# Kernel tuning notes

Measured on AMD Instinct MI355X. Metric: run time of the kernel, lower is better.

The kernel has to match this reference:

```python
import jax, jax.numpy as jnp
import numpy as np

B, S, D, H, FF = 1, 4096, 512, 8, 2048
DK = D // H
EPS = 1e-6


def layer_norm(x, alpha, beta):
    # Original LayerNorm: scalar alpha/beta, torch.std (ddof=1), eps added to std.
    mean = jnp.mean(x, axis=-1, keepdims=True)
    var = jnp.var(x, axis=-1, keepdims=True) * (D / (D - 1))  # Bessel-corrected, like torch.std
    std = jnp.sqrt(var)
    return alpha * (x - mean) / (std + EPS) + beta


def setup_inputs() -> dict:
    key = jax.random.key(0)
    ks = jax.random.split(key, 12)
    sd = 1.0 / np.sqrt(D)
    sf = 1.0 / np.sqrt(FF)
    inp = {
        "x": jax.random.normal(ks[0], (B, S, D), jnp.float32),
        "mask": jnp.ones((1, 1, 1, S), jnp.int32),
        "wq": jax.random.uniform(ks[1], (D, D), jnp.float32, -sd, sd),
        "bq": jnp.zeros((D,), jnp.float32),
        "wk": jax.random.uniform(ks[2], (D, D), jnp.float32, -sd, sd),
        "bk": jnp.zeros((D,), jnp.float32),
        "wv": jax.random.uniform(ks[3], (D, D), jnp.float32, -sd, sd),
        "bv": jnp.zeros((D,), jnp.float32),
        "wo": jax.random.uniform(ks[4], (D, D), jnp.float32, -sd, sd),
        "bo": jnp.zeros((D,), jnp.float32),
        "w1": jax.random.uniform(ks[5], (D, FF), jnp.float32, -sd, sd),
        "b1": jnp.zeros((FF,), jnp.float32),
        "w2": jax.random.uniform(ks[6], (FF, D), jnp.float32, -sf, sf),
        "b2": jnp.zeros((D,), jnp.float32),
        "ln1_a": jnp.ones((1,), jnp.float32),
        "ln1_b": jnp.zeros((1,), jnp.float32),
        "ln2_a": jnp.ones((1,), jnp.float32),
        "ln2_b": jnp.zeros((1,), jnp.float32),
    }
    return inp


def reference(x, mask, wq, bq, wk, bk, wv, bv, wo, bo, w1, b1, w2, b2,
              ln1_a, ln1_b, ln2_a, ln2_b):
    # --- pre-LN self-attention sublayer with residual ---
    h = layer_norm(x, ln1_a, ln1_b)
    q = (h @ wq + bq).reshape(B, S, H, DK).transpose(0, 2, 1, 3)  # [B,H,S,dk]
    k = (h @ wk + bk).reshape(B, S, H, DK).transpose(0, 2, 1, 3)
    v = (h @ wv + bv).reshape(B, S, H, DK).transpose(0, 2, 1, 3)
    scores = jnp.einsum('bhqd,bhkd->bhqk', q, k) / np.sqrt(DK)     # [B,H,S,S]
    scores = jnp.where(mask == 0, jnp.float32(-1e9), scores)
    probs = jax.nn.softmax(scores, axis=-1)
    attn = jnp.einsum('bhqk,bhkd->bhqd', probs, v)                 # [B,H,S,dk]
    attn = attn.transpose(0, 2, 1, 3).reshape(B, S, D)
    x = x + (attn @ wo + bo)
    # --- pre-LN feed-forward sublayer with residual ---
    h2 = layer_norm(x, ln2_a, ln2_b)
    ff = jax.nn.relu(h2 @ w1 + b1) @ w2 + b2
    return x + ff
```

## Files before the change

### kernel.cpp

```cpp
#include <hip/hip_runtime.h>
#include <hip/hip_bf16.h>

#define S_LEN 4096
#define D_DIM 512
#define H_NUM 8
#define DK_DIM 64
#define FF_DIM 2048
#define QLD 1536

typedef __attribute__((ext_vector_type(8))) short short8;
typedef __attribute__((ext_vector_type(4))) float f32x4;
typedef __attribute__((ext_vector_type(4))) ushort us4;

#if __has_builtin(__builtin_amdgcn_exp2f)
#define EXP2F __builtin_amdgcn_exp2f
#else
#define EXP2F exp2f
#endif

__device__ __forceinline__ ushort f2bf(float f) {
    union { float f; uint u; } v; v.f = f;
    uint r = v.u + 0x7FFF + ((v.u >> 16) & 1);
    return (ushort)(r >> 16);
}

__device__ __forceinline__ void gload_lds16(const void* g, void* l) {
    __builtin_amdgcn_global_load_lds(
        (const __attribute__((address_space(1))) void*)g,
        (__attribute__((address_space(3))) void*)l,
        16, 0, 0);
}

#define MFMA16(a, b, c) __builtin_amdgcn_mfma_f32_16x16x32_bf16(a, b, c, 0, 0, 0)

__global__ __launch_bounds__(256) void prep_all(
    const float* __restrict__ wq, const float* __restrict__ wk,
    const float* __restrict__ wv, const float* __restrict__ wo,
    const float* __restrict__ w1, const float* __restrict__ w2,
    const float* __restrict__ bq, const float* __restrict__ bk,
    const float* __restrict__ bv, const int* __restrict__ mask,
    ushort* __restrict__ wqkvt, ushort* __restrict__ wot,
    ushort* __restrict__ w1t, ushort* __restrict__ w2t,
    float* __restrict__ bqkv, float* __restrict__ mbias)
{
    __shared__ float t[32][33];
    const int bid = blockIdx.x, tid = threadIdx.x;
    if (bid < 3072) {
        const float* src; ushort* dst; int K, N, tx, ty;
        if (bid < 1024) {
            int wsel = bid >> 8, id = bid & 255;
            src = wsel == 0 ? wq : wsel == 1 ? wk : wsel == 2 ? wv : wo;
            dst = wsel == 0 ? wqkvt : wsel == 1 ? wqkvt + 512 * 512
                : wsel == 2 ? wqkvt + 1024 * 512 : wot;
            K = 512; N = 512; tx = id & 15; ty = id >> 4;
        } else if (bid < 2048) {
            int id = bid - 1024; src = w1; dst = w1t;
            K = 512; N = 2048; tx = id & 63; ty = id >> 6;
        } else {
            int id = bid - 2048; src = w2; dst = w2t;
            K = 2048; N = 512; tx = id & 15; ty = id >> 4;
        }
        int gn = tx * 32, gk = ty * 32;
        int lx = tid & 31, ly = tid >> 5;
#pragma unroll
        for (int i = 0; i < 32; i += 8)
            t[ly + i][lx] = src[(size_t)(gk + ly + i) * N + gn + lx];
        __syncthreads();
#pragma unroll
        for (int i = 0; i < 32; i += 8)
            dst[(size_t)(gn + ly + i) * K + gk + lx] = f2bf(t[lx][ly + i]);
    } else {
        int i = (bid - 3072) * 256 + tid;
        if (i < 512)       bqkv[i] = bq[i];
        else if (i < 1024) bqkv[i] = bk[i - 512];
        else if (i < 1536) bqkv[i] = bv[i - 1024];
        mbias[i] = mask[i] ? 0.0f : -1e9f;
    }
}

__global__ __launch_bounds__(256) void ln1_kernel(
    const float* __restrict__ x,
    const float* __restrict__ aP, const float* __restrict__ bP,
    ushort* __restrict__ out)
{
    const int row = blockIdx.x;
    const int d = threadIdx.x * 2;
    float2 v = *(const float2*)(x + (size_t)row * D_DIM + d);
    float sum = v.x + v.y;
    float sq  = v.x * v.x + v.y * v.y;
#pragma unroll
    for (int off = 1; off < 64; off <<= 1) {
        sum += __shfl_xor(sum, off);
        sq  += __shfl_xor(sq, off);
    }
    __shared__ float ssum[4], ssq[4];
    int wid = threadIdx.x >> 6;
    if ((threadIdx.x & 63) == 0) { ssum[wid] = sum; ssq[wid] = sq; }
    __syncthreads();
    sum = ssum[0] + ssum[1] + ssum[2] + ssum[3];
    sq  = ssq[0] + ssq[1] + ssq[2] + ssq[3];
    float mean = sum * (1.0f / D_DIM);
    float var  = (sq - (float)D_DIM * mean * mean) * (1.0f / (D_DIM - 1));
    var = fmaxf(var, 0.0f);
    float scale = aP[0] / (sqrtf(var) + 1e-6f);
    float beta  = bP[0];
    ushort2 o;
    o.x = f2bf((v.x - mean) * scale + beta);
    o.y = f2bf((v.y - mean) * scale + beta);
    *(ushort2*)(out + (size_t)row * D_DIM + d) = o;
}

__global__ __launch_bounds__(256) void ln2_fused(
    const float* __restrict__ x, const float* __restrict__ bo,
    const float* __restrict__ p0, const float* __restrict__ p1,
    const float* __restrict__ aP, const float* __restrict__ bP,
    float* __restrict__ x2, ushort* __restrict__ h2)
{
    const int row = blockIdx.x;
    const int d = threadIdx.x * 2;
    const size_t idx = (size_t)row * D_DIM + d;
    float2 xv = *(const float2*)(x + idx);
    float2 a0 = *(const float2*)(p0 + idx);
    float2 a1 = *(const float2*)(p1 + idx);
    float2 bb = *(const float2*)(bo + d);
    float2 v;
    v.x = xv.x + a0.x + a1.x + bb.x;
    v.y = xv.y + a0.y + a1.y + bb.y;
    *(float2*)(x2 + idx) = v;
    float sum = v.x + v.y;
    float sq  = v.x * v.x + v.y * v.y;
#pragma unroll
    for (int off = 1; off < 64; off <<= 1) {
        sum += __shfl_xor(sum, off);
        sq  += __shfl_xor(sq, off);
    }
    __shared__ float ssum[4], ssq[4];
    int wid = threadIdx.x >> 6;
    if ((threadIdx.x & 63) == 0) { ssum[wid] = sum; ssq[wid] = sq; }
    __syncthreads();
    sum = ssum[0] + ssum[1] + ssum[2] + ssum[3];
    sq  = ssq[0] + ssq[1] + ssq[2] + ssq[3];
    float mean = sum * (1.0f / D_DIM);
    float var  = (sq - (float)D_DIM * mean * mean) * (1.0f / (D_DIM - 1));
    var = fmaxf(var, 0.0f);
    float scale = aP[0] / (sqrtf(var) + 1e-6f);
    float beta  = bP[0];
    ushort2 o;
    o.x = f2bf((v.x - mean) * scale + beta);
    o.y = f2bf((v.y - mean) * scale + beta);
    *(ushort2*)(h2 + idx) = o;
}

__global__ __launch_bounds__(256) void gemm_mfma(
    const ushort* __restrict__ A, const ushort* __restrict__ Bt,
    const float* __restrict__ bias,
    float* __restrict__ outF, ushort* __restrict__ outB,
    ushort* __restrict__ outVT,
    int M, int N, int K, int relu, int ksl)
{
    __shared__ ushort As[2][2][128][32];
    __shared__ ushort Bs[2][2][64][32];
    const int tid = threadIdx.x;
    const int w = tid >> 6, lane = tid & 63;
    const int l15 = lane & 15, quad = lane >> 4;
    const int sw = (l15 >> 1) & 3;
    const int swc = ((lane & 3) ^ ((lane >> 3) & 3)) * 16;
    const int m0 = blockIdx.y * 128, n0 = blockIdx.x * 64;
    const int kz = blockIdx.z;
    const int kbeg = kz * ksl;

    f32x4 acc[2][4] = {};

    const char* gA  = (const char*)(A  + (size_t)(m0 + 32 * w + (lane >> 2)) * K + kbeg) + swc;
    const char* gA2 = gA + (size_t)16 * K * 2;
    const char* gB  = (const char*)(Bt + (size_t)(n0 + 16 * w + (lane >> 2)) * K + kbeg) + swc;

    auto stage = [&](int b) {
        gload_lds16(gA,       &As[b][0][32 * w][0]);
        gload_lds16(gA + 64,  &As[b][1][32 * w][0]);
        gload_lds16(gA2,      &As[b][0][32 * w + 16][0]);
        gload_lds16(gA2 + 64, &As[b][1][32 * w + 16][0]);
        gload_lds16(gB,       &Bs[b][0][16 * w][0]);
        gload_lds16(gB + 64,  &Bs[b][1][16 * w][0]);
        gA += 128; gA2 += 128; gB += 128;
    };

    stage(0);
    const int nit = ksl >> 6;
    for (int t = 0; t < nit; ++t) {
        __syncthreads();
        if (t + 1 < nit) stage((t + 1) & 1);
        const int b = t & 1;
#pragma unroll
        for (int ks = 0; ks < 2; ++ks) {
            short8 a0 = *(const short8*)&As[b][ks][32 * w + l15][(quad ^ sw) * 8];
            short8 a1 = *(const short8*)&As[b][ks][32 * w + 16 + l15][(quad ^ sw) * 8];
            short8 b0 = *(const short8*)&Bs[b][ks][0 * 16 + l15][(quad ^ sw) * 8];
            short8 b1 = *(const short8*)&Bs[b][ks][1 * 16 + l15][(quad ^ sw) * 8];
            short8 b2 = *(const short8*)&Bs[b][ks][2 * 16 + l15][(quad ^ sw) * 8];
            short8 b3 = *(const short8*)&Bs[b][ks][3 * 16 + l15][(quad ^ sw) * 8];
            acc[0][0] = MFMA16(a0, b0, acc[0][0]);
            acc[0][1] = MFMA16(a0, b1, acc[0][1]);
            acc[0][2] = MFMA16(a0, b2, acc[0][2]);
            acc[0][3] = MFMA16(a0, b3, acc[0][3]);
            acc[1][0] = MFMA16(a1, b0, acc[1][0]);
            acc[1][1] = MFMA16(a1, b1, acc[1][1]);
            acc[1][2] = MFMA16(a1, b2, acc[1][2]);
            acc[1][3] = MFMA16(a1, b3, acc[1][3]);
        }
    }

    if (ksl < K) {
        float* of = outF + (size_t)kz * M * N;
#pragma unroll
        for (int mt = 0; mt < 2; ++mt)
#pragma unroll
            for (int nt = 0; nt < 4; ++nt)
#pragma unroll
                for (int r = 0; r < 4; ++r) {
                    int mm = m0 + 32 * w + mt * 16 + quad * 4 + r;
                    int nn = n0 + nt * 16 + l15;
                    of[(size_t)mm * N + nn] = acc[mt][nt][r];
                }
        return;
    }

    if (outVT && n0 >= 1024) {
#pragma unroll
        for (int mt = 0; mt < 2; ++mt)
#pragma unroll
            for (int nt = 0; nt < 4; ++nt) {
                int nn = n0 + nt * 16 + l15;
                int mmb = m0 + 32 * w + mt * 16 + quad * 4;
                us4 pk;
#pragma unroll
                for (int r = 0; r < 4; ++r)
                    pk[r] = (short)f2bf(acc[mt][nt][r] + bias[nn]);
                *(us4*)(outVT + (size_t)(nn - 1024) * S_LEN + mmb) = pk;
            }
        return;
    }

    ushort (*Es)[32][68] = (ushort (*)[32][68])&As[0][0][0][0];
    __syncthreads();
#pragma unroll
    for (int mt = 0; mt < 2; ++mt)
#pragma unroll
        for (int nt = 0; nt < 4; ++nt)
#pragma unroll
            for (int r = 0; r < 4; ++r) {
                float v = acc[mt][nt][r] + bias[n0 + nt * 16 + l15];
                if (relu) v = fmaxf(v, 0.0f);
                Es[w][mt * 16 + quad * 4 + r][nt * 16 + l15] = f2bf(v);
            }
    __syncthreads();
#pragma unroll
    for (int p = 0; p < 4; ++p) {
        int row = p * 8 + (lane >> 3);
        int col = (lane & 7) * 8;
        short8 vv = *(const short8*)&Es[w][row][col];
        *(short8*)(outB + (size_t)(m0 + 32 * w + row) * N + n0 + col) = vv;
    }
}

__global__ __launch_bounds__(256, 2) void flash_mfma(
    const ushort* __restrict__ qkv, const ushort* __restrict__ vbt,
    const float* __restrict__ mbias, ushort* __restrict__ at_bf)
{
    __shared__ ushort Qs[2][64][32];
    __shared__ ushort Ks[2][128][32];
    __shared__ ushort Vt[4][64][32];
    __shared__ ushort Pld[4][64][40];

    const int bid = blockIdx.x;
    const int head = bid & 7;
    const int q0 = (bid >> 3) * 64;
    const int tid = threadIdx.x;
    const int w = tid >> 6, lane = tid & 63;
    const int l15 = lane & 15, quad = lane >> 4;
    const int hoff = head * DK_DIM;
    const int sw = (l15 >> 1) & 3;
    const int swc = ((lane & 3) ^ ((lane >> 3) & 3)) * 16;

    {
        const char* gq = (const char*)(qkv + (size_t)(q0 + 16 * w + (lane >> 2)) * QLD + hoff) + swc;
        gload_lds16(gq,      &Qs[0][16 * w][0]);
        gload_lds16(gq + 64, &Qs[1][16 * w][0]);
    }
    __syncthreads();
    short8 qf[2][4];
#pragma unroll
    for (int ks = 0; ks < 2; ++ks)
#pragma unroll
        for (int nt = 0; nt < 4; ++nt)
            qf[ks][nt] = *(const short8*)&Qs[ks][nt * 16 + l15][(quad ^ sw) * 8];

    const char* gk0 = (const char*)(qkv + (size_t)(32 * w + (lane >> 2)) * QLD + 512 + hoff) + swc;
    const char* gv0 = (const char*)(vbt + (size_t)(lane >> 2) * S_LEN + w * 32) + swc;

    const short8 ones = {0x3F80, 0x3F80, 0x3F80, 0x3F80,
                         0x3F80, 0x3F80, 0x3F80, 0x3F80};
    f32x4 oacc[4][4] = {};
    f32x4 lacc[4] = {};

    for (int t = 0; t < S_LEN / 128; ++t) {
        const int ktg = t * 128;
        __syncthreads();
        {
            const char* gk = gk0 + (size_t)ktg * (QLD * 2);
            gload_lds16(gk,                        &Ks[0][32 * w][0]);
            gload_lds16(gk + (size_t)16 * QLD * 2, &Ks[0][32 * w + 16][0]);
            gload_lds16(gk + 64,                   &Ks[1][32 * w][0]);
            gload_lds16(gk + (size_t)16 * QLD * 2 + 64, &Ks[1][32 * w + 16][0]);
            const char* gv = gv0 + ktg * 2;
            gload_lds16(gv,                          &Vt[w][0][0]);
            gload_lds16(gv + (size_t)16 * S_LEN * 2, &Vt[w][16][0]);
            gload_lds16(gv + (size_t)32 * S_LEN * 2, &Vt[w][32][0]);
            gload_lds16(gv + (size_t)48 * S_LEN * 2, &Vt[w][48][0]);
        }
        __syncthreads();

        f32x4 sacc[2][4] = {};
#pragma unroll
        for (int ks = 0; ks < 2; ++ks) {
            short8 kf0 = *(const short8*)&Ks[ks][32 * w + l15][(quad ^ sw) * 8];
            short8 kf1 = *(const short8*)&Ks[ks][32 * w + 16 + l15][(quad ^ sw) * 8];
#pragma unroll
            for (int nt = 0; nt < 4; ++nt) {
                sacc[0][nt] = MFMA16(kf0, qf[ks][nt], sacc[0][nt]);
                sacc[1][nt] = MFMA16(kf1, qf[ks][nt], sacc[1][nt]);
            }
        }

#pragma unroll
        for (int mt = 0; mt < 2; ++mt) {
            f32x4 mb = *(const f32x4*)&mbias[ktg + 32 * w + mt * 16 + quad * 4];
#pragma unroll
            for (int nt = 0; nt < 4; ++nt) {
                us4 pk;
#pragma unroll
                for (int r = 0; r < 4; ++r) {
                    float p = EXP2F(fmaf(sacc[mt][nt][r], 0.18033688011112042f, mb[r]));
                    pk[r] = (ushort)(__float_as_uint(p) >> 16);
                }
                *(us4*)&Pld[w][nt * 16 + l15][mt * 16 + quad * 4] = pk;
            }
        }

#pragma unroll
        for (int mt = 0; mt < 4; ++mt) {
            short8 ap = *(const short8*)&Pld[w][mt * 16 + l15][quad * 8];
            lacc[mt] = MFMA16(ap, ones, lacc[mt]);
#pragma unroll
            for (int nt = 0; nt < 4; ++nt) {
                short8 bv = *(const short8*)&Vt[w][nt * 16 + l15][(quad ^ sw) * 8];
                oacc[mt][nt] = MFMA16(ap, bv, oacc[mt][nt]);
            }
        }
    }

    float* Ored = (float*)&Pld[0][0][0];
    float* lred = (float*)&Qs[0][0][0];
    if (l15 == 0) {
#pragma unroll
        for (int mt = 0; mt < 4; ++mt)
#pragma unroll
            for (int r = 0; r < 4; ++r)
                lred[w * 64 + mt * 16 + quad * 4 + r] = lacc[mt][r];
    }
    const int qloc = tid >> 4, dk4 = (tid & 15) * 4;
#pragma unroll
    for (int mt = 0; mt < 4; ++mt) {
        __syncthreads();
#pragma unroll
        for (int nt = 0; nt < 4; ++nt)
#pragma unroll
            for (int r = 0; r < 4; ++r)
                Ored[(w * 16 + quad * 4 + r) * 68 + nt * 16 + l15] = oacc[mt][nt][r];
        __syncthreads();
        f32x4 s = *(const f32x4*)&Ored[(0 * 16 + qloc) * 68 + dk4];
#pragma unroll
        for (int ww = 1; ww < 4; ++ww) {
            f32x4 v = *(const f32x4*)&Ored[(ww * 16 + qloc) * 68 + dk4];
            s += v;
        }
        float l = lred[mt * 16 + qloc] + lred[64 + mt * 16 + qloc]
                + lred[128 + mt * 16 + qloc] + lred[192 + mt * 16 + qloc];
        float inv = 1.0f / l;
        us4 pk;
#pragma unroll
        for (int j = 0; j < 4; ++j) pk[j] = (short)f2bf(s[j] * inv);
        *(us4*)&at_bf[(size_t)(q0 + mt * 16 + qloc) * D_DIM + hoff + dk4] = pk;
    }
}

__global__ __launch_bounds__(256) void ff2_combine(
    const float* __restrict__ x2, const float* __restrict__ b2,
    const float* __restrict__ p0, const float* __restrict__ p1,
    float* __restrict__ out)
{
    size_t i = ((size_t)blockIdx.x * 256 + threadIdx.x) * 4;
    f32x4 a  = *(const f32x4*)(x2 + i);
    f32x4 q0 = *(const f32x4*)(p0 + i);
    f32x4 q1 = *(const f32x4*)(p1 + i);
    f32x4 bb = *(const f32x4*)(b2 + (int)(i & 511));
    f32x4 r = a + q0 + q1 + bb;
    *(f32x4*)(out + i) = r;
}

extern "C" void kernel_launch(void* const* d_in, const int* in_sizes, int n_in,
                              void* d_out, int out_size, void* d_ws, size_t ws_size,
                              hipStream_t stream) {
    (void)in_sizes; (void)n_in; (void)out_size; (void)ws_size;
    const float* x    = (const float*)d_in[0];
    const int*   mask = (const int*)d_in[1];
    const float* wq = (const float*)d_in[2];
    const float* bq = (const float*)d_in[3];
    const float* wk = (const float*)d_in[4];
    const float* bk = (const float*)d_in[5];
    const float* wv = (const float*)d_in[6];
    const float* bv = (const float*)d_in[7];
    const float* wo = (const float*)d_in[8];
    const float* bo = (const float*)d_in[9];
    const float* w1 = (const float*)d_in[10];
    const float* b1 = (const float*)d_in[11];
    const float* w2 = (const float*)d_in[12];
    const float* b2 = (const float*)d_in[13];
    const float* ln1a = (const float*)d_in[14];
    const float* ln1b = (const float*)d_in[15];
    const float* ln2a = (const float*)d_in[16];
    const float* ln2b = (const float*)d_in[17];
    float* out = (float*)d_out;

    const size_t SD = (size_t)S_LEN * D_DIM;
    char* p = (char*)d_ws;
    ushort* wqkvt = (ushort*)p; p += (size_t)1536 * 512 * 2;
    ushort* wot   = (ushort*)p; p += (size_t)512 * 512 * 2;
    ushort* w1t   = (ushort*)p; p += (size_t)2048 * 512 * 2;
    ushort* w2t   = (ushort*)p; p += (size_t)512 * 2048 * 2;
    float*  bqkv  = (float*)p;  p += 1536 * 4;
    float*  mbias = (float*)p;  p += 4096 * 4;
    ushort* h_bf  = (ushort*)p; p += SD * 2;
    ushort* qkv   = (ushort*)p; p += (size_t)4096 * 1536 * 2;
    ushort* vbt   = (ushort*)p; p += SD * 2;
    ushort* at_bf = (ushort*)p; p += SD * 2;
    float*  x2    = (float*)p;  p += SD * 4;
    ushort* h2    = (ushort*)p; p += SD * 2;
    ushort* ff1   = (ushort*)p; p += (size_t)4096 * 2048 * 2;
    float* wopart  = (float*)h_bf;
    float* ff2part = (float*)h_bf;

    dim3 blk(256);

    prep_all<<<dim3(3088), blk, 0, stream>>>(wq, wk, wv, wo, w1, w2, bq, bk, bv,
                                             mask, wqkvt, wot, w1t, w2t, bqkv, mbias);

    ln1_kernel<<<dim3(S_LEN), blk, 0, stream>>>(x, ln1a, ln1b, h_bf);

    gemm_mfma<<<dim3(24, 32, 1), blk, 0, stream>>>(
        h_bf, wqkvt, bqkv, nullptr, qkv, vbt, S_LEN, 1536, 512, 0, 512);

    flash_mfma<<<dim3(512), blk, 0, stream>>>(qkv, vbt, mbias, at_bf);

    gemm_mfma<<<dim3(8, 32, 2), blk, 0, stream>>>(
        at_bf, wot, nullptr, wopart, nullptr, nullptr, S_LEN, 512, 512, 0, 256);

    ln2_fused<<<dim3(S_LEN), blk, 0, stream>>>(x, bo, wopart, wopart + SD,
                                               ln2a, ln2b, x2, h2);

    gemm_mfma<<<dim3(32, 32, 1), blk, 0, stream>>>(
        h2, w1t, b1, nullptr, ff1, nullptr, S_LEN, 2048, 512, 1, 512);

    gemm_mfma<<<dim3(8, 32, 2), blk, 0, stream>>>(
        ff1, w2t, nullptr, ff2part, nullptr, nullptr, S_LEN, 512, 2048, 0, 1024);

    ff2_combine<<<dim3(2048), blk, 0, stream>>>(
        x2, b2, ff2part, ff2part + SD, out);
}
```

Before: 242.5 us.

## Add 128x128 GEMM tile kernel for QKV and FF1, slim flash attention LDS use

Adds a new gemm_mfma128 kernel with 128x128 tiles and a 2x2 warp layout (4x4 MFMA accumulators per warp) for the QKV projection and FF1 GEMMs. This raises operand reuse per LDS load and halves the number of blocks. The split-K gemm_mfma is reduced to a float-partial-only variant. In flash attention, Q fragments are loaded straight from global memory instead of staged through LDS, and V fragments are hoisted out of the inner loop. Score computation is split into two halves to cut live registers, and occupancy is raised to 3 blocks per CU. The trade-offs are higher register pressure in the larger-tile GEMM and uncoalesced direct Q loads.

```diff
diff --git a/kernel.cpp b/kernel.cpp
--- a/kernel.cpp
+++ b/kernel.cpp
@@ -151,12 +151,108 @@
     *(ushort2*)(h2 + idx) = o;
 }
 
+__global__ __launch_bounds__(256, 2) void gemm_mfma128(
+    const ushort* __restrict__ A, const ushort* __restrict__ Bt,
+    const float* __restrict__ bias,
+    ushort* __restrict__ outB, ushort* __restrict__ outVT,
+    int M, int N, int K, int relu)
+{
+    __shared__ ushort As[2][2][128][32];
+    __shared__ ushort Bs[2][2][128][32];
+    const int tid = threadIdx.x;
+    const int w = tid >> 6, lane = tid & 63;
+    const int l15 = lane & 15, quad = lane >> 4;
+    const int wm = w >> 1, wn = w & 1;
+    const int sw = (l15 >> 1) & 3;
+    const int swc = ((lane & 3) ^ ((lane >> 3) & 3)) * 16;
+    const int m0 = blockIdx.y * 128, n0 = blockIdx.x * 128;
+
+    f32x4 acc[4][4] = {};
+
+    const char* gA  = (const char*)(A  + (size_t)(m0 + 32 * w + (lane >> 2)) * K) + swc;
+    const char* gA2 = gA + (size_t)16 * K * 2;
+    const char* gB  = (const char*)(Bt + (size_t)(n0 + 32 * w + (lane >> 2)) * K) + swc;
+    const char* gB2 = gB + (size_t)16 * K * 2;
+
+    auto stage = [&](int b) {
+        gload_lds16(gA,       &As[b][0][32 * w][0]);
+        gload_lds16(gA + 64,  &As[b][1][32 * w][0]);
+        gload_lds16(gA2,      &As[b][0][32 * w + 16][0]);
+        gload_lds16(gA2 + 64, &As[b][1][32 * w + 16][0]);
+        gload_lds16(gB,       &Bs[b][0][32 * w][0]);
+        gload_lds16(gB + 64,  &Bs[b][1][32 * w][0]);
+        gload_lds16(gB2,      &Bs[b][0][32 * w + 16][0]);
+        gload_lds16(gB2 + 64, &Bs[b][1][32 * w + 16][0]);
+        gA += 128; gA2 += 128; gB += 128; gB2 += 128;
+    };
+
+    stage(0);
+    const int nit = K >> 6;
+    for (int t = 0; t < nit; ++t) {
+        __syncthreads();
+        if (t + 1 < nit) stage((t + 1) & 1);
+        const int b = t & 1;
+#pragma unroll
+        for (int ks = 0; ks < 2; ++ks) {
+            short8 af[4], bf[4];
+#pragma unroll
+            for (int i = 0; i < 4; ++i) {
+                af[i] = *(const short8*)&As[b][ks][64 * wm + i * 16 + l15][(quad ^ sw) * 8];
+                bf[i] = *(const short8*)&Bs[b][ks][64 * wn + i * 16 + l15][(quad ^ sw) * 8];
+            }
+#pragma unroll
+            for (int mt = 0; mt < 4; ++mt)
+#pragma unroll
+                for (int nt = 0; nt < 4; ++nt)
+                    acc[mt][nt] = MFMA16(af[mt], bf[nt], acc[mt][nt]);
+        }
+    }
+
+    if (outVT && n0 >= 1024) {
+#pragma unroll
+        for (int mt = 0; mt < 4; ++mt)
+#pragma unroll
+            for (int nt = 0; nt < 4; ++nt) {
+                int nn = n0 + 64 * wn + nt * 16 + l15;
+                int mmb = m0 + 64 * wm + mt * 16 + quad * 4;
+                us4 pk;
+#pragma unroll
+                for (int r = 0; r < 4; ++r)
+                    pk[r] = (short)f2bf(acc[mt][nt][r] + bias[nn]);
+                *(us4*)(outVT + (size_t)(nn - 1024) * S_LEN + mmb) = pk;
+            }
+        return;
+    }
+
+    ushort (*Es)[32][68] = (ushort (*)[32][68])&As[0][0][0][0];
+    __syncthreads();
+#pragma unroll
+    for (int h = 0; h < 2; ++h) {
+#pragma unroll
+        for (int mt = 2 * h; mt < 2 * h + 2; ++mt)
+#pragma unroll
+            for (int nt = 0; nt < 4; ++nt)
+#pragma unroll
+                for (int r = 0; r < 4; ++r) {
+                    float v = acc[mt][nt][r] + bias[n0 + 64 * wn + nt * 16 + l15];
+                    if (relu) v = fmaxf(v, 0.0f);
+                    Es[w][(mt & 1) * 16 + quad * 4 + r][nt * 16 + l15] = f2bf(v);
+                }
+#pragma unroll
+        for (int p2 = 0; p2 < 4; ++p2) {
+            int row = p2 * 8 + (lane >> 3);
+            int col = (lane & 7) * 8;
+            short8 vv = *(const short8*)&Es[w][row][col];
+            *(short8*)(outB + (size_t)(m0 + 64 * wm + h * 32 + row) * N
+                             + n0 + 64 * wn + col) = vv;
+        }
+    }
+}
+
 __global__ __launch_bounds__(256) void gemm_mfma(
     const ushort* __restrict__ A, const ushort* __restrict__ Bt,
-    const float* __restrict__ bias,
-    float* __restrict__ outF, ushort* __restrict__ outB,
-    ushort* __restrict__ outVT,
-    int M, int N, int K, int relu, int ksl)
+    float* __restrict__ outF,
+    int M, int N, int K, int ksl)
 {
     __shared__ ushort As[2][2][128][32];
     __shared__ ushort Bs[2][2][64][32];
@@ -210,64 +306,23 @@
         }
     }
 
-    if (ksl < K) {
-        float* of = outF + (size_t)kz * M * N;
-#pragma unroll
-        for (int mt = 0; mt < 2; ++mt)
-#pragma unroll
-            for (int nt = 0; nt < 4; ++nt)
-#pragma unroll
-                for (int r = 0; r < 4; ++r) {
-                    int mm = m0 + 32 * w + mt * 16 + quad * 4 + r;
-                    int nn = n0 + nt * 16 + l15;
-                    of[(size_t)mm * N + nn] = acc[mt][nt][r];
-                }
-        return;
-    }
-
-    if (outVT && n0 >= 1024) {
-#pragma unroll
-        for (int mt = 0; mt < 2; ++mt)
-#pragma unroll
-            for (int nt = 0; nt < 4; ++nt) {
+    float* of = outF + (size_t)kz * M * N;
+#pragma unroll
+    for (int mt = 0; mt < 2; ++mt)
+#pragma unroll
+        for (int nt = 0; nt < 4; ++nt)
+#pragma unroll
+            for (int r = 0; r < 4; ++r) {
+                int mm = m0 + 32 * w + mt * 16 + quad * 4 + r;
                 int nn = n0 + nt * 16 + l15;
-                int mmb = m0 + 32 * w + mt * 16 + quad * 4;
-                us4 pk;
-#pragma unroll
-                for (int r = 0; r < 4; ++r)
-                    pk[r] = (short)f2bf(acc[mt][nt][r] + bias[nn]);
-                *(us4*)(outVT + (size_t)(nn - 1024) * S_LEN + mmb) = pk;
+                of[(size_t)mm * N + nn] = acc[mt][nt][r];
             }
-        return;
-    }
-
-    ushort (*Es)[32][68] = (ushort (*)[32][68])&As[0][0][0][0];
-    __syncthreads();
-#pragma unroll
-    for (int mt = 0; mt < 2; ++mt)
-#pragma unroll
-        for (int nt = 0; nt < 4; ++nt)
-#pragma unroll
-            for (int r = 0; r < 4; ++r) {
-                float v = acc[mt][nt][r] + bias[n0 + nt * 16 + l15];
-                if (relu) v = fmaxf(v, 0.0f);
-                Es[w][mt * 16 + quad * 4 + r][nt * 16 + l15] = f2bf(v);
-            }
-    __syncthreads();
-#pragma unroll
-    for (int p = 0; p < 4; ++p) {
-        int row = p * 8 + (lane >> 3);
-        int col = (lane & 7) * 8;
-        short8 vv = *(const short8*)&Es[w][row][col];
-        *(short8*)(outB + (size_t)(m0 + 32 * w + row) * N + n0 + col) = vv;
-    }
-}
-
-__global__ __launch_bounds__(256, 2) void flash_mfma(
+}
+
+__global__ __launch_bounds__(256, 3) void flash_mfma(
     const ushort* __restrict__ qkv, const ushort* __restrict__ vbt,
     const float* __restrict__ mbias, ushort* __restrict__ at_bf)
 {
-    __shared__ ushort Qs[2][64][32];
     __shared__ ushort Ks[2][128][32];
     __shared__ ushort Vt[4][64][32];
     __shared__ ushort Pld[4][64][40];
@@ -282,18 +337,13 @@
     const int sw = (l15 >> 1) & 3;
     const int swc = ((lane & 3) ^ ((lane >> 3) & 3)) * 16;
 
-    {
-        const char* gq = (const char*)(qkv + (size_t)(q0 + 16 * w + (lane >> 2)) * QLD + hoff) + swc;
-        gload_lds16(gq,      &Qs[0][16 * w][0]);
-        gload_lds16(gq + 64, &Qs[1][16 * w][0]);
-    }
-    __syncthreads();
     short8 qf[2][4];
 #pragma unroll
     for (int ks = 0; ks < 2; ++ks)
 #pragma unroll
         for (int nt = 0; nt < 4; ++nt)
-            qf[ks][nt] = *(const short8*)&Qs[ks][nt * 16 + l15][(quad ^ sw) * 8];
+            qf[ks][nt] = *(const short8*)(qkv
+                + (size_t)(q0 + nt * 16 + l15) * QLD + hoff + ks * 32 + quad * 8);
 
     const char* gk0 = (const char*)(qkv + (size_t)(32 * w + (lane >> 2)) * QLD + 512 + hoff) + swc;
     const char* gv0 = (const char*)(vbt + (size_t)(lane >> 2) * S_LEN + w * 32) + swc;
@@ -308,9 +358,9 @@
         __syncthreads();
         {
             const char* gk = gk0 + (size_t)ktg * (QLD * 2);
-            gload_lds16(gk,                        &Ks[0][32 * w][0]);
-            gload_lds16(gk + (size_t)16 * QLD * 2, &Ks[0][32 * w + 16][0]);
-            gload_lds16(gk + 64,                   &Ks[1][32 * w][0]);
+            gload_lds16(gk,                             &Ks[0][32 * w][0]);
+            gload_lds16(gk + (size_t)16 * QLD * 2,      &Ks[0][32 * w + 16][0]);
+            gload_lds16(gk + 64,                        &Ks[1][32 * w][0]);
             gload_lds16(gk + (size_t)16 * QLD * 2 + 64, &Ks[1][32 * w + 16][0]);
             const char* gv = gv0 + ktg * 2;
             gload_lds16(gv,                          &Vt[w][0][0]);
@@ -320,70 +370,66 @@
         }
         __syncthreads();
 
-        f32x4 sacc[2][4] = {};
-#pragma unroll
-        for (int ks = 0; ks < 2; ++ks) {
-            short8 kf0 = *(const short8*)&Ks[ks][32 * w + l15][(quad ^ sw) * 8];
-            short8 kf1 = *(const short8*)&Ks[ks][32 * w + 16 + l15][(quad ^ sw) * 8];
-#pragma unroll
-            for (int nt = 0; nt < 4; ++nt) {
-                sacc[0][nt] = MFMA16(kf0, qf[ks][nt], sacc[0][nt]);
-                sacc[1][nt] = MFMA16(kf1, qf[ks][nt], sacc[1][nt]);
+#pragma unroll
+        for (int kh = 0; kh < 2; ++kh) {
+            f32x4 sacc[4] = {};
+#pragma unroll
+            for (int ks = 0; ks < 2; ++ks) {
+                short8 kf = *(const short8*)&Ks[ks][32 * w + kh * 16 + l15][(quad ^ sw) * 8];
+#pragma unroll
+                for (int nt = 0; nt < 4; ++nt)
+                    sacc[nt] = MFMA16(kf, qf[ks][nt], sacc[nt]);
             }
-        }
-
-#pragma unroll
-        for (int mt = 0; mt < 2; ++mt) {
-            f32x4 mb = *(const f32x4*)&mbias[ktg + 32 * w + mt * 16 + quad * 4];
+            f32x4 mb = *(const f32x4*)&mbias[ktg + 32 * w + kh * 16 + quad * 4];
 #pragma unroll
             for (int nt = 0; nt < 4; ++nt) {
                 us4 pk;
 #pragma unroll
                 for (int r = 0; r < 4; ++r) {
-                    float p = EXP2F(fmaf(sacc[mt][nt][r], 0.18033688011112042f, mb[r]));
-                    pk[r] = (ushort)(__float_as_uint(p) >> 16);
+                    float pv = EXP2F(fmaf(sacc[nt][r], 0.18033688011112042f, mb[r]));
+                    pk[r] = (ushort)(__float_as_uint(pv) >> 16);
                 }
-                *(us4*)&Pld[w][nt * 16 + l15][mt * 16 + quad * 4] = pk;
+                *(us4*)&Pld[w][nt * 16 + l15][kh * 16 + quad * 4] = pk;
             }
         }
 
+        short8 bvr[4];
+#pragma unroll
+        for (int nt = 0; nt < 4; ++nt)
+            bvr[nt] = *(const short8*)&Vt[w][nt * 16 + l15][(quad ^ sw) * 8];
 #pragma unroll
         for (int mt = 0; mt < 4; ++mt) {
             short8 ap = *(const short8*)&Pld[w][mt * 16 + l15][quad * 8];
             lacc[mt] = MFMA16(ap, ones, lacc[mt]);
 #pragma unroll
-            for (int nt = 0; nt < 4; ++nt) {
-                short8 bv = *(const short8*)&Vt[w][nt * 16 + l15][(quad ^ sw) * 8];
-                oacc[mt][nt] = MFMA16(ap, bv, oacc[mt][nt]);
-            }
+            for (int nt = 0; nt < 4; ++nt)
+                oacc[mt][nt] = MFMA16(ap, bvr[nt], oacc[mt][nt]);
         }
     }
 
     float* Ored = (float*)&Pld[0][0][0];
-    float* lred = (float*)&Qs[0][0][0];
-    if (l15 == 0) {
-#pragma unroll
-        for (int mt = 0; mt < 4; ++mt)
-#pragma unroll
-            for (int r = 0; r < 4; ++r)
-                lred[w * 64 + mt * 16 + quad * 4 + r] = lacc[mt][r];
-    }
+    float* lred = (float*)&Ks[0][0][0];
     const int qloc = tid >> 4, dk4 = (tid & 15) * 4;
 #pragma unroll
     for (int mt = 0; mt < 4; ++mt) {
         __syncthreads();
+        if (mt == 0 && l15 == 0) {
+#pragma unroll
+            for (int m2 = 0; m2 < 4; ++m2)
+#pragma unroll
+                for (int r = 0; r < 4; ++r)
+                    lred[w * 64 + m2 * 16 + quad * 4 + r] = lacc[m2][r];
+        }
 #pragma unroll
         for (int nt = 0; nt < 4; ++nt)
 #pragma unroll
             for (int r = 0; r < 4; ++r)
                 Ored[(w * 16 + quad * 4 + r) * 68 + nt * 16 + l15] = oacc[mt][nt][r];
         __syncthreads();
-        f32x4 s = *(const f32x4*)&Ored[(0 * 16 + qloc) * 68 + dk4];
-#pragma unroll
-        for (int ww = 1; ww < 4; ++ww) {
-            f32x4 v = *(const f32x4*)&Ored[(ww * 16 + qloc) * 68 + dk4];
-            s += v;
-        }
+        f32x4 s = *(const f32x4*)&Ored[qloc * 68 + dk4];
+#pragma unroll
+        for (int ww = 1; ww < 4; ++ww)
+            s += *(const f32x4*)&Ored[(ww * 16 + qloc) * 68 + dk4];
         float l = lred[mt * 16 + qloc] + lred[64 + mt * 16 + qloc]
                 + lred[128 + mt * 16 + qloc] + lred[192 + mt * 16 + qloc];
         float inv = 1.0f / l;
@@ -457,22 +503,22 @@
 
     ln1_kernel<<<dim3(S_LEN), blk, 0, stream>>>(x, ln1a, ln1b, h_bf);
 
-    gemm_mfma<<<dim3(24, 32, 1), blk, 0, stream>>>(
-        h_bf, wqkvt, bqkv, nullptr, qkv, vbt, S_LEN, 1536, 512, 0, 512);
+    gemm_mfma128<<<dim3(12, 32), blk, 0, stream>>>(
+        h_bf, wqkvt, bqkv, qkv, vbt, S_LEN, 1536, 512, 0);
 
     flash_mfma<<<dim3(512), blk, 0, stream>>>(qkv, vbt, mbias, at_bf);
 
     gemm_mfma<<<dim3(8, 32, 2), blk, 0, stream>>>(
-        at_bf, wot, nullptr, wopart, nullptr, nullptr, S_LEN, 512, 512, 0, 256);
+        at_bf, wot, wopart, S_LEN, 512, 512, 256);
 
     ln2_fused<<<dim3(S_LEN), blk, 0, stream>>>(x, bo, wopart, wopart + SD,
                                                ln2a, ln2b, x2, h2);
 
-    gemm_mfma<<<dim3(32, 32, 1), blk, 0, stream>>>(
-        h2, w1t, b1, nullptr, ff1, nullptr, S_LEN, 2048, 512, 1, 512);
+    gemm_mfma128<<<dim3(16, 32), blk, 0, stream>>>(
+        h2, w1t, b1, ff1, nullptr, S_LEN, 2048, 512, 1);
 
     gemm_mfma<<<dim3(8, 32, 2), blk, 0, stream>>>(
-        ff1, w2t, nullptr, ff2part, nullptr, nullptr, S_LEN, 512, 2048, 0, 1024);
+        ff1, w2t, ff2part, S_LEN, 512, 2048, 1024);
 
     ff2_combine<<<dim3(2048), blk, 0, stream>>>(
         x2, b2, ff2part, ff2part + SD, out);
```

New measurement: 245.6 us. About the same (+1.3%).
